# Optimization experiments

Measured on AMD Instinct MI355X. Metric: run time of the kernel, lower is better.

The kernel has to match this reference:

```python
import jax, jax.numpy as jnp
import numpy as np

N_U, N_V = 8192, 8192
IN_U, IN_V = 64, 64
OUT_U, OUT_V = 64, 64
RATING = 5


def setup_inputs() -> dict:
    key = jax.random.key(0)
    k1, k2, k3, k4, k5 = jax.random.split(key, 5)
    adj = jax.random.randint(k1, (N_U, N_V), 0, 6, dtype=jnp.int32)  # ratings 0..5, 0 = no edge
    u_feature = jax.random.normal(k2, (N_U, IN_U), dtype=jnp.float32)
    v_feature = jax.random.normal(k3, (N_V, IN_V), dtype=jnp.float32)
    weight_u = 0.02 * jax.random.normal(k4, (RATING, IN_V, OUT_U), dtype=jnp.float32)
    weight_v = 0.02 * jax.random.normal(k5, (RATING, IN_U, OUT_V), dtype=jnp.float32)
    return {"adj": adj, "u_feature": u_feature, "v_feature": v_feature,
            "weight_u": weight_u, "weight_v": weight_v}


def reference(adj, u_feature, v_feature, weight_u, weight_v):
    rating = weight_u.shape[0]
    dt = u_feature.dtype
    # Per-rating binary masks M_r: [R, n_u, n_v]
    ratings = jnp.arange(1, rating + 1, dtype=adj.dtype)
    masks = (adj[None, :, :] == ratings[:, None, None]).astype(dt)
    # Degree normalization (reciprocal of nonzero counts; inf -> 0)
    deg_u = jnp.sum(adj > 0, axis=1).astype(dt)  # [n_u]
    deg_v = jnp.sum(adj > 0, axis=0).astype(dt)  # [n_v]
    d_u = jnp.where(deg_u > 0, 1.0 / deg_u, 0.0)
    d_v = jnp.where(deg_v > 0, 1.0 / deg_v, 0.0)
    # Aggregate neighbor features per rating, project, sum over ratings.
    agg_u = jnp.einsum('ruv,vf->ruf', masks, v_feature)      # [R, n_u, in_v]
    out_u = jnp.einsum('ruf,rfo->uo', agg_u, weight_u)        # [n_u, out_u]
    out_u = d_u[:, None] * out_u
    agg_v = jnp.einsum('ruv,uf->rvf', masks, u_feature)      # [R, n_v, in_u]
    out_v = jnp.einsum('rvf,rfo->vo', agg_v, weight_v)        # [n_v, out_v]
    out_v = d_v[:, None] * out_v
    return (jax.nn.relu(out_u), jax.nn.relu(out_v))
```

## Files before the change

kernel.cpp:

```cpp
#include <hip/hip_runtime.h>

#define N_U 8192
#define N_V 8192
#define DIM 64
#define NR 5
#define BM 256
#define BK 512
#define NSTEP 16

typedef __attribute__((ext_vector_type(8))) short short8;
typedef __attribute__((ext_vector_type(4))) float f32x4;

__device__ inline unsigned short f2bf(float x) {
    unsigned u = __float_as_uint(x);
    return (unsigned short)((u + 0x7FFFu + ((u >> 16) & 1u)) >> 16);
}

__device__ inline size_t pfrag_idx(int r, int k, int o) {
    int ktile = k >> 5;
    int g     = (k >> 3) & 3;
    int j     = k & 7;
    int lane  = g * 16 + (o & 15);
    int n     = o >> 4;
    return ((((size_t)r * (N_V / 32) + ktile) * 4 + n) * 64 + lane) * 8 + j;
}

__global__ __launch_bounds__(256) void precompute_P(
    const float* __restrict__ u_feat, const float* __restrict__ v_feat,
    const float* __restrict__ w_u, const float* __restrict__ w_v,
    unsigned short* __restrict__ p_u, unsigned short* __restrict__ p_v)
{
    int wid  = (blockIdx.x * blockDim.x + threadIdx.x) >> 6;
    int lane = threadIdx.x & 63;
    const int tasks = 2 * NR * (N_V / 32);
    if (wid >= tasks) return;
    int dir  = wid / (NR * (N_V / 32));
    int rem  = wid % (NR * (N_V / 32));
    int r    = rem / (N_V / 32);
    int v0   = (rem % (N_V / 32)) * 32;

    const float* feat = dir ? u_feat : v_feat;
    const float* w    = dir ? w_v : w_u;
    unsigned short* dst = dir ? p_v : p_u;

    float wreg[DIM];
#pragma unroll
    for (int f = 0; f < DIM; ++f) wreg[f] = w[(r * DIM + f) * DIM + lane];

    for (int v = v0; v < v0 + 32; ++v) {
        float x = feat[(size_t)v * DIM + lane];
        float acc = 0.f;
#pragma unroll
        for (int f = 0; f < DIM; ++f) acc += __shfl(x, f) * wreg[f];
        dst[pfrag_idx(r, v, lane)] = f2bf(acc);
    }
}

template <int TRANS>
__global__ __launch_bounds__(512, 4) void gemm_masked(
    const int* __restrict__ adj, const unsigned short* __restrict__ pfrag,
    float* __restrict__ outp, unsigned int* __restrict__ deg)
{
    __shared__ unsigned char tile[BM][256];
    __shared__ unsigned int  cnt[BM];

    const int tid  = threadIdx.x;
    const int lane = tid & 63;
    const int wv   = tid >> 6;
    const int b0   = blockIdx.x * BM;
    const int k0   = blockIdx.y * BK;

    unsigned cpack = 0;

    if (TRANS == 0) {
        int4 pre[4], nxt[4];
        const int sub = tid & 31;
        auto issue = [&](int rnd, int4* dst) {
            int row = rnd * 16 + (tid >> 5);
            const int* base = adj + (size_t)(b0 + row) * N_V + k0 + sub * 4;
#pragma unroll
            for (int it = 0; it < 4; ++it) dst[it] = *(const int4*)(base + it * 128);
        };
        issue(0, pre);
        for (int rnd = 0; rnd < 16; ++rnd) {
            if (rnd + 1 < 16) issue(rnd + 1, nxt);
            int row = rnd * 16 + (tid >> 5);
            unsigned lo = 0, hi = 0;
#pragma unroll
            for (int it = 0; it < 4; ++it) {
                int4 a = pre[it];
                unsigned long long bx = __ballot(a.x != 0), by = __ballot(a.y != 0);
                unsigned long long bz = __ballot(a.z != 0), bw = __ballot(a.w != 0);
                lo += __popcll(bx & 0xFFFFFFFFull) + __popcll(by & 0xFFFFFFFFull) +
                      __popcll(bz & 0xFFFFFFFFull) + __popcll(bw & 0xFFFFFFFFull);
                hi += __popcll(bx >> 32) + __popcll(by >> 32) +
                      __popcll(bz >> 32) + __popcll(bw >> 32);
                unsigned pk = (unsigned)a.x | ((unsigned)a.y << 4) |
                              ((unsigned)a.z << 8) | ((unsigned)a.w << 12);
                int d  = it * 16 + (sub >> 1);
                int dp = d ^ (row & 31);
                *(unsigned short*)&tile[row][dp * 4 + (sub & 1) * 2] = (unsigned short)pk;
            }
            if ((tid & 31) == 0) cnt[row] = (lane & 32) ? hi : lo;
#pragma unroll
            for (int it = 0; it < 4; ++it) pre[it] = nxt[it];
        }
    } else {
        const int v4 = (tid & 63) * 4;
        int4 pre[4], nxt[4];
        auto issue = [&](int rnd, int4* dst) {
            int u0 = rnd * 32 + (tid >> 6) * 4;
#pragma unroll
            for (int c = 0; c < 4; ++c)
                dst[c] = *(const int4*)(adj + (size_t)(k0 + u0 + c) * N_V + b0 + v4);
        };
        issue(0, pre);
        for (int rnd = 0; rnd < 16; ++rnd) {
            if (rnd + 1 < 16) issue(rnd + 1, nxt);
            const int* q0 = (const int*)&pre[0]; const int* q1 = (const int*)&pre[1];
            const int* q2 = (const int*)&pre[2]; const int* q3 = (const int*)&pre[3];
            int d    = rnd * 4 + ((tid >> 6) >> 1);
            int half = (tid >> 6) & 1;
#pragma unroll
            for (int cc = 0; cc < 4; ++cc) {
                int x0 = q0[cc], x1 = q1[cc], x2 = q2[cc], x3 = q3[cc];
                unsigned pk = (unsigned)x0 | ((unsigned)x1 << 4) |
                              ((unsigned)x2 << 8) | ((unsigned)x3 << 12);
                int row = v4 + cc;
                int dp  = d ^ (row & 31);
                *(unsigned short*)&tile[row][dp * 4 + half * 2] = (unsigned short)pk;
                cpack += (unsigned)((x0 != 0) + (x1 != 0) + (x2 != 0) + (x3 != 0)) << (8 * cc);
            }
#pragma unroll
            for (int c = 0; c < 4; ++c) pre[c] = nxt[c];
        }
    }
    __syncthreads();

    f32x4 acc[2][4];
#pragma unroll
    for (int m = 0; m < 2; ++m)
#pragma unroll
        for (int n = 0; n < 4; ++n) acc[m][n] = (f32x4){0.f, 0.f, 0.f, 0.f};

    const int mrow = wv * 32;
    for (int s = 0; s < NSTEP; ++s) {
        unsigned nib[2];
#pragma unroll
        for (int m = 0; m < 2; ++m) {
            int row = mrow + m * 16 + (lane & 15);
            int d   = s * 4 + (lane >> 4);
            nib[m] = *(const unsigned*)&tile[row][((d ^ (row & 31)) << 2)];
        }
        const int ktg = (k0 >> 5) + s;
#pragma unroll
        for (int r = 0; r < NR; ++r) {
            short8 bf[4];
#pragma unroll
            for (int n = 0; n < 4; ++n)
                bf[n] = *(const short8*)(pfrag +
                         ((((size_t)r * (N_V / 32) + ktg) * 4 + n) * 64 + lane) * 8);
            short8 am[2];
#pragma unroll
            for (int m = 0; m < 2; ++m)
#pragma unroll
                for (int j = 0; j < 8; ++j) {
                    unsigned nb = (nib[m] >> (4 * j)) & 0xFu;
                    am[m][j] = (short)(nb == (unsigned)(r + 1) ? 0x3F80 : 0);
                }
#pragma unroll
            for (int n = 0; n < 4; ++n) {
                acc[0][n] = __builtin_amdgcn_mfma_f32_16x16x32_bf16(am[0], bf[n], acc[0][n], 0, 0, 0);
                acc[1][n] = __builtin_amdgcn_mfma_f32_16x16x32_bf16(am[1], bf[n], acc[1][n], 0, 0, 0);
            }
        }
    }

#pragma unroll
    for (int m = 0; m < 2; ++m) {
        int rbase = b0 + mrow + m * 16 + ((lane >> 4) << 2);
#pragma unroll
        for (int n = 0; n < 4; ++n)
#pragma unroll
            for (int q = 0; q < 4; ++q)
                atomicAdd(&outp[(size_t)(rbase + q) * DIM + n * 16 + (lane & 15)], acc[m][n][q]);
    }

    if (TRANS == 0) {
        if (tid < BM) atomicAdd(&deg[b0 + tid], cnt[tid]);
    } else {
        __syncthreads();
        unsigned* sc = (unsigned*)&tile[0][0];
        sc[tid] = cpack;
        __syncthreads();
        if (tid < BM) {
            unsigned tot = 0;
            int base = tid >> 2, byte = tid & 3;
#pragma unroll
            for (int j = 0; j < 8; ++j) tot += (sc[j * 64 + base] >> (8 * byte)) & 0xFFu;
            atomicAdd(&deg[b0 + tid], tot);
        }
    }
}

__global__ __launch_bounds__(256) void finalize_k(
    float* __restrict__ outp, const unsigned int* __restrict__ deg_u,
    const unsigned int* __restrict__ deg_v)
{
    int idx = blockIdx.x * blockDim.x + threadIdx.x;
    const int total = 2 * N_U * DIM;
    for (; idx < total; idx += gridDim.x * blockDim.x) {
        int row = idx >> 6;
        unsigned d = (row < N_U) ? deg_u[row] : deg_v[row - N_U];
        float s = d ? (1.f / (float)d) : 0.f;
        float v = outp[idx] * s;
        outp[idx] = v > 0.f ? v : 0.f;
    }
}

extern "C" void kernel_launch(void* const* d_in, const int* in_sizes, int n_in,
                              void* d_out, int out_size, void* d_ws, size_t ws_size,
                              hipStream_t stream)
{
    const int*   adj = (const int*)d_in[0];
    const float* uf  = (const float*)d_in[1];
    const float* vf  = (const float*)d_in[2];
    const float* wu  = (const float*)d_in[3];
    const float* wv  = (const float*)d_in[4];
    float* outp = (float*)d_out;

    unsigned char* ws = (unsigned char*)d_ws;
    const size_t P_BYTES = (size_t)NR * (N_V / 32) * 4 * 64 * 8 * 2;
    unsigned short* p_u   = (unsigned short*)ws;
    unsigned short* p_v   = (unsigned short*)(ws + P_BYTES);
    unsigned int*   deg_u = (unsigned int*)(ws + 2 * P_BYTES);
    unsigned int*   deg_v = (unsigned int*)(ws + 2 * P_BYTES + N_U * sizeof(unsigned int));

    hipMemsetAsync(d_out, 0, (size_t)2 * N_U * DIM * sizeof(float), stream);
    hipMemsetAsync(ws + 2 * P_BYTES, 0, (N_U + N_V) * sizeof(unsigned int), stream);

    precompute_P<<<640, 256, 0, stream>>>(uf, vf, wu, wv, p_u, p_v);

    dim3 grid(N_U / BM, N_V / BK);
    gemm_masked<0><<<grid, 512, 0, stream>>>(adj, p_u, outp, deg_u);
    gemm_masked<1><<<grid, 512, 0, stream>>>(adj, p_v, outp + (size_t)N_U * DIM, deg_v);

    finalize_k<<<2048, 256, 0, stream>>>(outp, deg_u, deg_v);
}
```

Baseline: 286.0 us.

## Fuse both masked GEMM directions into one kernel sharing the adjacency tile

After: 270.5 us. -5.4%, faster.

```diff
diff --git a/kernel.cpp b/kernel.cpp
--- a/kernel.cpp
+++ b/kernel.cpp
@@ -6,7 +6,6 @@
 #define NR 5
 #define BM 256
 #define BK 512
-#define NSTEP 16
 
 typedef __attribute__((ext_vector_type(8))) short short8;
 typedef __attribute__((ext_vector_type(4))) float f32x4;
@@ -23,6 +22,16 @@
     int lane  = g * 16 + (o & 15);
     int n     = o >> 4;
     return ((((size_t)r * (N_V / 32) + ktile) * 4 + n) * 64 + lane) * 8 + j;
+}
+
+__global__ __launch_bounds__(256) void zero_k(float* __restrict__ outp,
+                                              unsigned* __restrict__ deg)
+{
+    const int stride = gridDim.x * blockDim.x;
+    int i = blockIdx.x * blockDim.x + threadIdx.x;
+    int4 z = {0, 0, 0, 0};
+    for (int idx = i; idx < 2 * N_U * DIM / 4; idx += stride) ((int4*)outp)[idx] = z;
+    for (int idx = i; idx < (N_U + N_V) / 4; idx += stride) ((int4*)deg)[idx] = z;
 }
 
 __global__ __launch_bounds__(256) void precompute_P(
@@ -56,25 +65,29 @@
     }
 }
 
-template <int TRANS>
-__global__ __launch_bounds__(512, 4) void gemm_masked(
-    const int* __restrict__ adj, const unsigned short* __restrict__ pfrag,
+__global__ __launch_bounds__(512, 4) void gemm_fused(
+    const int* __restrict__ adj,
+    const unsigned short* __restrict__ p_u, const unsigned short* __restrict__ p_v,
     float* __restrict__ outp, unsigned int* __restrict__ deg)
 {
     __shared__ unsigned char tile[BM][256];
-    __shared__ unsigned int  cnt[BM];
+    __shared__ unsigned int  cnt_u[BM];
+    __shared__ unsigned int  scv[512][4];
 
     const int tid  = threadIdx.x;
     const int lane = tid & 63;
     const int wv   = tid >> 6;
     const int b0   = blockIdx.x * BM;
     const int k0   = blockIdx.y * BK;
-
-    unsigned cpack = 0;
-
-    if (TRANS == 0) {
+    float* out_u = outp;
+    float* out_v = outp + (size_t)N_U * DIM;
+    unsigned* deg_u = deg;
+    unsigned* deg_v = deg + N_U;
+
+    {
         int4 pre[4], nxt[4];
         const int sub = tid & 31;
+        unsigned cv[4] = {0, 0, 0, 0};
         auto issue = [&](int rnd, int4* dst) {
             int row = rnd * 16 + (tid >> 5);
             const int* base = adj + (size_t)(b0 + row) * N_V + k0 + sub * 4;
@@ -95,111 +108,143 @@
                       __popcll(bz & 0xFFFFFFFFull) + __popcll(bw & 0xFFFFFFFFull);
                 hi += __popcll(bx >> 32) + __popcll(by >> 32) +
                       __popcll(bz >> 32) + __popcll(bw >> 32);
+                cv[it] += (unsigned)(a.x != 0) | ((unsigned)(a.y != 0) << 8) |
+                          ((unsigned)(a.z != 0) << 16) | ((unsigned)(a.w != 0) << 24);
                 unsigned pk = (unsigned)a.x | ((unsigned)a.y << 4) |
                               ((unsigned)a.z << 8) | ((unsigned)a.w << 12);
                 int d  = it * 16 + (sub >> 1);
                 int dp = d ^ (row & 31);
                 *(unsigned short*)&tile[row][dp * 4 + (sub & 1) * 2] = (unsigned short)pk;
             }
-            if ((tid & 31) == 0) cnt[row] = (lane & 32) ? hi : lo;
+            if ((tid & 31) == 0) cnt_u[row] = (lane & 32) ? hi : lo;
 #pragma unroll
             for (int it = 0; it < 4; ++it) pre[it] = nxt[it];
         }
-    } else {
-        const int v4 = (tid & 63) * 4;
-        int4 pre[4], nxt[4];
-        auto issue = [&](int rnd, int4* dst) {
-            int u0 = rnd * 32 + (tid >> 6) * 4;
-#pragma unroll
-            for (int c = 0; c < 4; ++c)
-                dst[c] = *(const int4*)(adj + (size_t)(k0 + u0 + c) * N_V + b0 + v4);
-        };
-        issue(0, pre);
-        for (int rnd = 0; rnd < 16; ++rnd) {
-            if (rnd + 1 < 16) issue(rnd + 1, nxt);
-            const int* q0 = (const int*)&pre[0]; const int* q1 = (const int*)&pre[1];
-            const int* q2 = (const int*)&pre[2]; const int* q3 = (const int*)&pre[3];
-            int d    = rnd * 4 + ((tid >> 6) >> 1);
-            int half = (tid >> 6) & 1;
-#pragma unroll
-            for (int cc = 0; cc < 4; ++cc) {
-                int x0 = q0[cc], x1 = q1[cc], x2 = q2[cc], x3 = q3[cc];
-                unsigned pk = (unsigned)x0 | ((unsigned)x1 << 4) |
-                              ((unsigned)x2 << 8) | ((unsigned)x3 << 12);
-                int row = v4 + cc;
-                int dp  = d ^ (row & 31);
-                *(unsigned short*)&tile[row][dp * 4 + half * 2] = (unsigned short)pk;
-                cpack += (unsigned)((x0 != 0) + (x1 != 0) + (x2 != 0) + (x3 != 0)) << (8 * cc);
-            }
-#pragma unroll
-            for (int c = 0; c < 4; ++c) pre[c] = nxt[c];
-        }
+#pragma unroll
+        for (int it = 0; it < 4; ++it) scv[tid][it] = cv[it];
     }
     __syncthreads();
 
-    f32x4 acc[2][4];
-#pragma unroll
-    for (int m = 0; m < 2; ++m)
-#pragma unroll
-        for (int n = 0; n < 4; ++n) acc[m][n] = (f32x4){0.f, 0.f, 0.f, 0.f};
-
-    const int mrow = wv * 32;
-    for (int s = 0; s < NSTEP; ++s) {
-        unsigned nib[2];
+    const unsigned* t32 = (const unsigned*)&tile[0][0];
+
+    {
+        f32x4 acc[2][4];
+#pragma unroll
+        for (int m = 0; m < 2; ++m)
+#pragma unroll
+            for (int n = 0; n < 4; ++n) acc[m][n] = (f32x4){0.f, 0.f, 0.f, 0.f};
+
+        const int mrow = wv * 32;
+        for (int s = 0; s < 16; ++s) {
+            unsigned nib[2];
+#pragma unroll
+            for (int m = 0; m < 2; ++m) {
+                int row = mrow + m * 16 + (lane & 15);
+                int d   = s * 4 + (lane >> 4);
+                nib[m] = t32[row * 64 + (d ^ (row & 31))];
+            }
+            const int ktg = (k0 >> 5) + s;
+#pragma unroll
+            for (int r = 0; r < NR; ++r) {
+                short8 bf[4];
+#pragma unroll
+                for (int n = 0; n < 4; ++n)
+                    bf[n] = *(const short8*)(p_u +
+                             ((((size_t)r * (N_V / 32) + ktg) * 4 + n) * 64 + lane) * 8);
+                short8 am[2];
+#pragma unroll
+                for (int m = 0; m < 2; ++m)
+#pragma unroll
+                    for (int j = 0; j < 8; ++j)
+                        am[m][j] = (short)(((nib[m] >> (4 * j)) & 0xFu) == (unsigned)(r + 1) ? 0x3F80 : 0);
+#pragma unroll
+                for (int n = 0; n < 4; ++n) {
+                    acc[0][n] = __builtin_amdgcn_mfma_f32_16x16x32_bf16(am[0], bf[n], acc[0][n], 0, 0, 0);
+                    acc[1][n] = __builtin_amdgcn_mfma_f32_16x16x32_bf16(am[1], bf[n], acc[1][n], 0, 0, 0);
+                }
+            }
+        }
 #pragma unroll
         for (int m = 0; m < 2; ++m) {
-            int row = mrow + m * 16 + (lane & 15);
-            int d   = s * 4 + (lane >> 4);
-            nib[m] = *(const unsigned*)&tile[row][((d ^ (row & 31)) << 2)];
-        }
-        const int ktg = (k0 >> 5) + s;
-#pragma unroll
-        for (int r = 0; r < NR; ++r) {
-            short8 bf[4];
+            int rbase = b0 + mrow + m * 16 + ((lane >> 4) << 2);
 #pragma unroll
             for (int n = 0; n < 4; ++n)
-                bf[n] = *(const short8*)(pfrag +
-                         ((((size_t)r * (N_V / 32) + ktg) * 4 + n) * 64 + lane) * 8);
-            short8 am[2];
-#pragma unroll
-            for (int m = 0; m < 2; ++m)
-#pragma unroll
-                for (int j = 0; j < 8; ++j) {
-                    unsigned nb = (nib[m] >> (4 * j)) & 0xFu;
-                    am[m][j] = (short)(nb == (unsigned)(r + 1) ? 0x3F80 : 0);
+#pragma unroll
+                for (int q = 0; q < 4; ++q)
+                    atomicAdd(&out_u[(size_t)(rbase + q) * DIM + n * 16 + (lane & 15)], acc[m][n][q]);
+        }
+    }
+
+    {
+        f32x4 acc[4][4];
+#pragma unroll
+        for (int m = 0; m < 4; ++m)
+#pragma unroll
+            for (int n = 0; n < 4; ++n) acc[m][n] = (f32x4){0.f, 0.f, 0.f, 0.f};
+
+        const int g = lane >> 4;
+        int cd[4], sh[4];
+#pragma unroll
+        for (int m = 0; m < 4; ++m) {
+            int c = wv * 64 + m * 16 + (lane & 15);
+            cd[m] = c >> 3;
+            sh[m] = 4 * (c & 7);
+        }
+
+        for (int kt = 0; kt < 8; ++kt) {
+            unsigned nbp[4] = {0, 0, 0, 0};
+#pragma unroll
+            for (int j = 0; j < 8; ++j) {
+                int row = kt * 32 + g * 8 + j;
+                int rx  = row & 31;
+#pragma unroll
+                for (int m = 0; m < 4; ++m) {
+                    unsigned dw = t32[row * 64 + (cd[m] ^ rx)];
+                    nbp[m] |= ((dw >> sh[m]) & 0xFu) << (4 * j);
                 }
-#pragma unroll
-            for (int n = 0; n < 4; ++n) {
-                acc[0][n] = __builtin_amdgcn_mfma_f32_16x16x32_bf16(am[0], bf[n], acc[0][n], 0, 0, 0);
-                acc[1][n] = __builtin_amdgcn_mfma_f32_16x16x32_bf16(am[1], bf[n], acc[1][n], 0, 0, 0);
-            }
-        }
-    }
-
-#pragma unroll
-    for (int m = 0; m < 2; ++m) {
-        int rbase = b0 + mrow + m * 16 + ((lane >> 4) << 2);
-#pragma unroll
-        for (int n = 0; n < 4; ++n)
-#pragma unroll
-            for (int q = 0; q < 4; ++q)
-                atomicAdd(&outp[(size_t)(rbase + q) * DIM + n * 16 + (lane & 15)], acc[m][n][q]);
-    }
-
-    if (TRANS == 0) {
-        if (tid < BM) atomicAdd(&deg[b0 + tid], cnt[tid]);
-    } else {
-        __syncthreads();
-        unsigned* sc = (unsigned*)&tile[0][0];
-        sc[tid] = cpack;
-        __syncthreads();
-        if (tid < BM) {
-            unsigned tot = 0;
-            int base = tid >> 2, byte = tid & 3;
-#pragma unroll
-            for (int j = 0; j < 8; ++j) tot += (sc[j * 64 + base] >> (8 * byte)) & 0xFFu;
-            atomicAdd(&deg[b0 + tid], tot);
-        }
+            }
+            const int ktg = (b0 >> 5) + kt;
+#pragma unroll
+            for (int r = 0; r < NR; ++r) {
+                short8 bf[4];
+#pragma unroll
+                for (int n = 0; n < 4; ++n)
+                    bf[n] = *(const short8*)(p_v +
+                             ((((size_t)r * (N_U / 32) + ktg) * 4 + n) * 64 + lane) * 8);
+#pragma unroll
+                for (int m = 0; m < 4; ++m) {
+                    short8 am;
+#pragma unroll
+                    for (int j = 0; j < 8; ++j)
+                        am[j] = (short)(((nbp[m] >> (4 * j)) & 0xFu) == (unsigned)(r + 1) ? 0x3F80 : 0);
+#pragma unroll
+                    for (int n = 0; n < 4; ++n)
+                        acc[m][n] = __builtin_amdgcn_mfma_f32_16x16x32_bf16(am, bf[n], acc[m][n], 0, 0, 0);
+                }
+            }
+        }
+#pragma unroll
+        for (int m = 0; m < 4; ++m) {
+            int rbase = k0 + wv * 64 + m * 16 + ((lane >> 4) << 2);
+#pragma unroll
+            for (int n = 0; n < 4; ++n)
+#pragma unroll
+                for (int q = 0; q < 4; ++q)
+                    atomicAdd(&out_v[(size_t)(rbase + q) * DIM + n * 16 + (lane & 15)], acc[m][n][q]);
+        }
+    }
+
+    if (tid < BM) atomicAdd(&deg_u[b0 + tid], cnt_u[tid]);
+    {
+        int c   = tid;
+        int it  = c >> 7;
+        int sub = (c & 127) >> 2;
+        int q   = c & 3;
+        unsigned tot = 0;
+#pragma unroll
+        for (int rg = 0; rg < 16; ++rg)
+            tot += (scv[rg * 32 + sub][it] >> (8 * q)) & 0xFFu;
+        atomicAdd(&deg_v[k0 + c], tot);
     }
 }
 
@@ -231,19 +276,15 @@
 
     unsigned char* ws = (unsigned char*)d_ws;
     const size_t P_BYTES = (size_t)NR * (N_V / 32) * 4 * 64 * 8 * 2;
-    unsigned short* p_u   = (unsigned short*)ws;
-    unsigned short* p_v   = (unsigned short*)(ws + P_BYTES);
-    unsigned int*   deg_u = (unsigned int*)(ws + 2 * P_BYTES);
-    unsigned int*   deg_v = (unsigned int*)(ws + 2 * P_BYTES + N_U * sizeof(unsigned int));
-
-    hipMemsetAsync(d_out, 0, (size_t)2 * N_U * DIM * sizeof(float), stream);
-    hipMemsetAsync(ws + 2 * P_BYTES, 0, (N_U + N_V) * sizeof(unsigned int), stream);
-
+    unsigned short* p_u = (unsigned short*)ws;
+    unsigned short* p_v = (unsigned short*)(ws + P_BYTES);
+    unsigned int*   deg = (unsigned int*)(ws + 2 * P_BYTES);
+
+    zero_k<<<1024, 256, 0, stream>>>(outp, deg);
     precompute_P<<<640, 256, 0, stream>>>(uf, vf, wu, wv, p_u, p_v);
 
     dim3 grid(N_U / BM, N_V / BK);
-    gemm_masked<0><<<grid, 512, 0, stream>>>(adj, p_u, outp, deg_u);
-    gemm_masked<1><<<grid, 512, 0, stream>>>(adj, p_v, outp + (size_t)N_U * DIM, deg_v);
-
-    finalize_k<<<2048, 256, 0, stream>>>(outp, deg_u, deg_v);
-}
+    gemm_fused<<<grid, 512, 0, stream>>>(adj, p_u, p_v, outp, deg);
+
+    finalize_k<<<2048, 256, 0, stream>>>(outp, deg, deg + N_U);
+}
```

## Split K across wave halves with 64-row M tiles and LDS reduction

Applied to the files above, without the earlier changes.

Result: slower. 577.5 us (+101.9%).

```diff
diff --git a/kernel.cpp b/kernel.cpp
--- a/kernel.cpp
+++ b/kernel.cpp
@@ -1,12 +1,10 @@
 #include <hip/hip_runtime.h>
 
-#define N_U 8192
-#define N_V 8192
+#define NN 8192
 #define DIM 64
 #define NR 5
 #define BM 256
 #define BK 512
-#define NSTEP 16
 
 typedef __attribute__((ext_vector_type(8))) short short8;
 typedef __attribute__((ext_vector_type(4))) float f32x4;
@@ -16,13 +14,23 @@
     return (unsigned short)((u + 0x7FFFu + ((u >> 16) & 1u)) >> 16);
 }
 
-__device__ inline size_t pfrag_idx(int r, int k, int o) {
+__device__ inline int pfrag_idx(int r, int k, int o) {
     int ktile = k >> 5;
     int g     = (k >> 3) & 3;
     int j     = k & 7;
     int lane  = g * 16 + (o & 15);
     int n     = o >> 4;
-    return ((((size_t)r * (N_V / 32) + ktile) * 4 + n) * 64 + lane) * 8 + j;
+    return ((r * (NN / 32) + ktile) * 4 + n) * 512 + lane * 8 + j;
+}
+
+__global__ __launch_bounds__(256) void zero_k(float* __restrict__ outp,
+                                              unsigned* __restrict__ deg)
+{
+    const int stride = gridDim.x * blockDim.x;
+    int i = blockIdx.x * blockDim.x + threadIdx.x;
+    int4 z = {0, 0, 0, 0};
+    for (int idx = i; idx < 2 * NN * DIM / 4; idx += stride) ((int4*)outp)[idx] = z;
+    for (int idx = i; idx < 2 * NN / 4; idx += stride) ((int4*)deg)[idx] = z;
 }
 
 __global__ __launch_bounds__(256) void precompute_P(
@@ -32,12 +40,12 @@
 {
     int wid  = (blockIdx.x * blockDim.x + threadIdx.x) >> 6;
     int lane = threadIdx.x & 63;
-    const int tasks = 2 * NR * (N_V / 32);
+    const int tasks = 2 * NR * (NN / 32);
     if (wid >= tasks) return;
-    int dir  = wid / (NR * (N_V / 32));
-    int rem  = wid % (NR * (N_V / 32));
-    int r    = rem / (N_V / 32);
-    int v0   = (rem % (N_V / 32)) * 32;
+    int dir  = wid / (NR * (NN / 32));
+    int rem  = wid % (NR * (NN / 32));
+    int r    = rem / (NN / 32);
+    int v0   = (rem % (NN / 32)) * 32;
 
     const float* feat = dir ? u_feat : v_feat;
     const float* w    = dir ? w_v : w_u;
@@ -63,6 +71,7 @@
 {
     __shared__ unsigned char tile[BM][256];
     __shared__ unsigned int  cnt[BM];
+    __shared__ unsigned int  sc2[512];
 
     const int tid  = threadIdx.x;
     const int lane = tid & 63;
@@ -77,7 +86,7 @@
         const int sub = tid & 31;
         auto issue = [&](int rnd, int4* dst) {
             int row = rnd * 16 + (tid >> 5);
-            const int* base = adj + (size_t)(b0 + row) * N_V + k0 + sub * 4;
+            const int* base = adj + (size_t)(b0 + row) * NN + k0 + sub * 4;
 #pragma unroll
             for (int it = 0; it < 4; ++it) dst[it] = *(const int4*)(base + it * 128);
         };
@@ -112,7 +121,7 @@
             int u0 = rnd * 32 + (tid >> 6) * 4;
 #pragma unroll
             for (int c = 0; c < 4; ++c)
-                dst[c] = *(const int4*)(adj + (size_t)(k0 + u0 + c) * N_V + b0 + v4);
+                dst[c] = *(const int4*)(adj + (size_t)(k0 + u0 + c) * NN + b0 + v4);
         };
         issue(0, pre);
         for (int rnd = 0; rnd < 16; ++rnd) {
@@ -134,23 +143,29 @@
 #pragma unroll
             for (int c = 0; c < 4; ++c) pre[c] = nxt[c];
         }
+        sc2[tid] = cpack;
     }
     __syncthreads();
 
-    f32x4 acc[2][4];
-#pragma unroll
-    for (int m = 0; m < 2; ++m)
+    const unsigned* t32 = (const unsigned*)&tile[0][0];
+    const int mgrp = wv & 3;
+    const int ph   = wv >> 2;
+    const int g    = lane >> 4;
+    const int c15  = lane & 15;
+
+    f32x4 acc[4][4];
+#pragma unroll
+    for (int m = 0; m < 4; ++m)
 #pragma unroll
         for (int n = 0; n < 4; ++n) acc[m][n] = (f32x4){0.f, 0.f, 0.f, 0.f};
 
-    const int mrow = wv * 32;
-    for (int s = 0; s < NSTEP; ++s) {
-        unsigned nib[2];
-#pragma unroll
-        for (int m = 0; m < 2; ++m) {
-            int row = mrow + m * 16 + (lane & 15);
-            int d   = s * 4 + (lane >> 4);
-            nib[m] = *(const unsigned*)&tile[row][((d ^ (row & 31)) << 2)];
+    for (int s = ph; s < 16; s += 2) {
+        unsigned nib[4];
+#pragma unroll
+        for (int m = 0; m < 4; ++m) {
+            int row = mgrp * 64 + m * 16 + c15;
+            int d   = s * 4 + g;
+            nib[m] = t32[row * 64 + (d ^ (row & 31))];
         }
         const int ktg = (k0 >> 5) + s;
 #pragma unroll
@@ -159,45 +174,54 @@
 #pragma unroll
             for (int n = 0; n < 4; ++n)
                 bf[n] = *(const short8*)(pfrag +
-                         ((((size_t)r * (N_V / 32) + ktg) * 4 + n) * 64 + lane) * 8);
-            short8 am[2];
-#pragma unroll
-            for (int m = 0; m < 2; ++m)
-#pragma unroll
-                for (int j = 0; j < 8; ++j) {
-                    unsigned nb = (nib[m] >> (4 * j)) & 0xFu;
-                    am[m][j] = (short)(nb == (unsigned)(r + 1) ? 0x3F80 : 0);
+                         ((size_t)(r * (NN / 32) + ktg) * 4 + n) * 512 + lane * 8);
+#pragma unroll
+            for (int m = 0; m < 4; ++m) {
+                short8 am;
+#pragma unroll
+                for (int j = 0; j < 8; ++j)
+                    am[j] = (short)(((nib[m] >> (4 * j)) & 0xFu) == (unsigned)(r + 1) ? 0x3F80 : 0);
+#pragma unroll
+                for (int n = 0; n < 4; ++n)
+                    acc[m][n] = __builtin_amdgcn_mfma_f32_16x16x32_bf16(am, bf[n], acc[m][n], 0, 0, 0);
+            }
+        }
+    }
+
+    __syncthreads();
+    float* lf = (float*)&tile[0][0];
+    if (wv >= 4) {
+#pragma unroll
+        for (int m = 0; m < 4; ++m)
+#pragma unroll
+            for (int n = 0; n < 4; ++n)
+#pragma unroll
+                for (int q = 0; q < 4; ++q)
+                    lf[(mgrp * 64 + m * 16 + g * 4 + q) * 64 + ((n ^ g) * 16 + c15)] = acc[m][n][q];
+    }
+    __syncthreads();
+    if (wv < 4) {
+#pragma unroll
+        for (int m = 0; m < 4; ++m) {
+#pragma unroll
+            for (int n = 0; n < 4; ++n)
+#pragma unroll
+                for (int q = 0; q < 4; ++q) {
+                    int rl = mgrp * 64 + m * 16 + g * 4 + q;
+                    float sum = acc[m][n][q] + lf[rl * 64 + ((n ^ g) * 16 + c15)];
+                    atomicAdd(&outp[(size_t)(b0 + rl) * DIM + n * 16 + c15], sum);
                 }
-#pragma unroll
-            for (int n = 0; n < 4; ++n) {
-                acc[0][n] = __builtin_amdgcn_mfma_f32_16x16x32_bf16(am[0], bf[n], acc[0][n], 0, 0, 0);
-                acc[1][n] = __builtin_amdgcn_mfma_f32_16x16x32_bf16(am[1], bf[n], acc[1][n], 0, 0, 0);
-            }
-        }
-    }
-
-#pragma unroll
-    for (int m = 0; m < 2; ++m) {
-        int rbase = b0 + mrow + m * 16 + ((lane >> 4) << 2);
-#pragma unroll
-        for (int n = 0; n < 4; ++n)
-#pragma unroll
-            for (int q = 0; q < 4; ++q)
-                atomicAdd(&outp[(size_t)(rbase + q) * DIM + n * 16 + (lane & 15)], acc[m][n][q]);
+        }
     }
 
     if (TRANS == 0) {
         if (tid < BM) atomicAdd(&deg[b0 + tid], cnt[tid]);
     } else {
-        __syncthreads();
-        unsigned* sc = (unsigned*)&tile[0][0];
-        sc[tid] = cpack;
-        __syncthreads();
         if (tid < BM) {
             unsigned tot = 0;
             int base = tid >> 2, byte = tid & 3;
 #pragma unroll
-            for (int j = 0; j < 8; ++j) tot += (sc[j * 64 + base] >> (8 * byte)) & 0xFFu;
+            for (int j = 0; j < 8; ++j) tot += (sc2[j * 64 + base] >> (8 * byte)) & 0xFFu;
             atomicAdd(&deg[b0 + tid], tot);
         }
     }
@@ -208,10 +232,10 @@
     const unsigned int* __restrict__ deg_v)
 {
     int idx = blockIdx.x * blockDim.x + threadIdx.x;
-    const int total = 2 * N_U * DIM;
+    const int total = 2 * NN * DIM;
     for (; idx < total; idx += gridDim.x * blockDim.x) {
         int row = idx >> 6;
-        unsigned d = (row < N_U) ? deg_u[row] : deg_v[row - N_U];
+        unsigned d = (row < NN) ? deg_u[row] : deg_v[row - NN];
         float s = d ? (1.f / (float)d) : 0.f;
         float v = outp[idx] * s;
         outp[idx] = v > 0.f ? v : 0.f;
@@ -230,20 +254,17 @@
     float* outp = (float*)d_out;
 
     unsigned char* ws = (unsigned char*)d_ws;
-    const size_t P_BYTES = (size_t)NR * (N_V / 32) * 4 * 64 * 8 * 2;
-    unsigned short* p_u   = (unsigned short*)ws;
-    unsigned short* p_v   = (unsigned short*)(ws + P_BYTES);
-    unsigned int*   deg_u = (unsigned int*)(ws + 2 * P_BYTES);
-    unsigned int*   deg_v = (unsigned int*)(ws + 2 * P_BYTES + N_U * sizeof(unsigned int));
-
-    hipMemsetAsync(d_out, 0, (size_t)2 * N_U * DIM * sizeof(float), stream);
-    hipMemsetAsync(ws + 2 * P_BYTES, 0, (N_U + N_V) * sizeof(unsigned int), stream);
-
+    const size_t P_BYTES = (size_t)NR * (NN / 32) * 4 * 64 * 8 * 2;
+    unsigned short* p_u = (unsigned short*)ws;
+    unsigned short* p_v = (unsigned short*)(ws + P_BYTES);
+    unsigned int*   deg = (unsigned int*)(ws + 2 * P_BYTES);
+
+    zero_k<<<1024, 256, 0, stream>>>(outp, deg);
     precompute_P<<<640, 256, 0, stream>>>(uf, vf, wu, wv, p_u, p_v);
 
-    dim3 grid(N_U / BM, N_V / BK);
-    gemm_masked<0><<<grid, 512, 0, stream>>>(adj, p_u, outp, deg_u);
-    gemm_masked<1><<<grid, 512, 0, stream>>>(adj, p_v, outp + (size_t)N_U * DIM, deg_v);
-
-    finalize_k<<<2048, 256, 0, stream>>>(outp, deg_u, deg_v);
-}
+    dim3 grid(NN / BM, NN / BK);
+    gemm_masked<0><<<grid, 512, 0, stream>>>(adj, p_u, outp, deg);
+    gemm_masked<1><<<grid, 512, 0, stream>>>(adj, p_v, outp + (size_t)NN * DIM, deg + NN);
+
+    finalize_k<<<2048, 256, 0, stream>>>(outp, deg, deg + NN);
+}
```
